# Kernel tuning notes

Hardware: AMD Instinct MI355X
Metric: run time of the kernel (lower is better)

## Reference

```python
import jax, jax.numpy as jnp
import numpy as np

M = 150        # AR2 tail-fit window
LAM = 1e-3     # ridge regularizer in the 2x2 solve
CLIP_K = 4.0   # soft clip multiplier
H = 96         # forecast horizon (base_model.H)


def setup_inputs() -> dict:
    key = jax.random.key(0)
    k1, k2 = jax.random.split(key)
    x = jax.random.normal(k1, (32, 512, 2048), dtype=jnp.float32)
    W = jax.random.normal(k2, (2048, 96), dtype=jnp.float32) * 0.02
    return {"x": x, "W": W}


def _ar2_forecast(x):
    # x: (B, C, L); closed-form AR2 fit on last M samples, vectorized over (B, C)
    y = x[..., -M:]                     # (B, C, M)
    Y = y[..., 2:]                      # targets
    p1 = y[..., 1:-1]
    p2 = y[..., :-2]
    s = lambda a, b: jnp.sum(a * b, axis=-1)
    A11 = s(p1, p1) + LAM
    A22 = s(p2, p2) + LAM
    A12 = s(p1, p2)
    b1 = s(p1, Y)
    b2 = s(p2, Y)
    det = A11 * A22 - A12 * A12
    a1 = (b1 * A22 - b2 * A12) / det    # (B, C)
    a2 = (A11 * b2 - A12 * b1) / det

    def step(carry, _):
        y1, y2 = carry
        yn = a1 * y1 + a2 * y2
        return (yn, y1), yn

    _, out = jax.lax.scan(step, (x[..., -1], x[..., -2]), None, length=H)
    return jnp.moveaxis(out, 0, -1)     # (B, C, H)


def reference(x, W):
    # AR2 part is computed on detached history in the original (numpy round-trip)
    Yb = jax.lax.stop_gradient(_ar2_forecast(x))
    d_hat = jnp.einsum('bcl,lh->bch', x, W)          # base model: per-channel linear head
    y_hat = Yb + d_hat
    last = x[..., -1:]                               # (B, C, 1), broadcasts over H
    hstd = jnp.maximum(jnp.std(x, axis=-1, ddof=1, keepdims=True), 1e-6)  # torch unbiased std
    return jnp.clip(y_hat, last - CLIP_K * hstd, last + CLIP_K * hstd)
```

## Files before the change

kernel.cpp:

```cpp
#include <hip/hip_runtime.h>
#include <math.h>

constexpr int L     = 2048;
constexpr int NH    = 96;
constexpr int MLEN  = 150;
constexpr int NAR   = 148;
constexpr float LAM    = 0.001f;
constexpr float CLIP_K = 4.0f;

constexpr int TM     = 64;
constexpr int KM     = 64;
constexpr int MSTEPS = L / KM;

typedef __attribute__((ext_vector_type(8))) short short8;
typedef __attribute__((ext_vector_type(4))) float floatx4;

__device__ inline short f2bf(float f) {
    union { float f; unsigned u; } v; v.f = f;
    unsigned r = v.u + 0x7FFFu + ((v.u >> 16) & 1u);
    return (short)(r >> 16);
}

__global__ __launch_bounds__(256) void wt_kernel(
    const float* __restrict__ W, short* __restrict__ Wt)
{
    int idx = blockIdx.x * 256 + threadIdx.x;
    int n = idx >> 11;
    int k = idx & 2047;
    Wt[idx] = f2bf(W[k * NH + n]);
}

__global__ __launch_bounds__(512) void gemm_ar2_kernel(
    const float* __restrict__ x, const short* __restrict__ Wt,
    float* __restrict__ out)
{
    __shared__ float As[2][TM * KM];
    __shared__ short Bs[2][NH * KM];
    __shared__ float los[TM], his[TM];

    const int t    = threadIdx.x;
    const int lane = t & 63;
    const int wv   = t >> 6;
    const int h    = wv >> 1;
    const int g    = wv & 1;
    const int m    = lane & 15;
    const int quad = lane >> 4;
    const int row0 = blockIdx.x * TM;
    const int r    = h * 16 + m;
    const int m7   = m & 7;

    const int cA0 = (wv * 2) * 64 + lane, cA1 = cA0 + 64;
    const int rA0 = cA0 >> 4, chA0 = cA0 & 15;
    const int rA1 = cA1 >> 4, chA1 = cA1 & 15;
    const float* pa0 = x + (size_t)(row0 + rA0) * L
                         + ((chA0 >> 3) * 32 + ((chA0 & 7) ^ (rA0 & 7)) * 4);
    const float* pa1 = x + (size_t)(row0 + rA1) * L
                         + ((chA1 >> 3) * 32 + ((chA1 & 7) ^ (rA1 & 7)) * 4);

    const int cB0 = wv * 64 + lane;
    const int cB1 = (8 + wv) * 64 + lane;
    const short* pb0 = Wt + (size_t)(cB0 >> 3) * L + (((cB0 & 7) ^ ((cB0 >> 3) & 7)) * 8);
    const short* pb1 = Wt + (size_t)(cB1 >> 3) * L + (((cB1 & 7) ^ ((cB1 >> 3) & 7)) * 8);

    floatx4 acc[3];
    #pragma unroll
    for (int jj = 0; jj < 3; ++jj) acc[jj] = floatx4{0.f, 0.f, 0.f, 0.f};
    float sum = 0.f, sumsq = 0.f;

    auto stage = [&](int buf, int k0) {
        __builtin_amdgcn_global_load_lds(
            (const __attribute__((address_space(1))) unsigned int*)(pa0 + k0),
            (__attribute__((address_space(3))) unsigned int*)&As[buf][(wv * 2) * 256], 16, 0, 0);
        __builtin_amdgcn_global_load_lds(
            (const __attribute__((address_space(1))) unsigned int*)(pa1 + k0),
            (__attribute__((address_space(3))) unsigned int*)&As[buf][(wv * 2 + 1) * 256], 16, 0, 0);
        __builtin_amdgcn_global_load_lds(
            (const __attribute__((address_space(1))) unsigned int*)(pb0 + k0),
            (__attribute__((address_space(3))) unsigned int*)&Bs[buf][wv * 512], 16, 0, 0);
        if (wv < 4)
            __builtin_amdgcn_global_load_lds(
                (const __attribute__((address_space(1))) unsigned int*)(pb1 + k0),
                (__attribute__((address_space(3))) unsigned int*)&Bs[buf][(8 + wv) * 512], 16, 0, 0);
    };

    stage(0, 0);

    const int pA0 = (2 * quad) ^ m7, pA1 = (2 * quad + 1) ^ m7;

    for (int s = 0; s < MSTEPS; ++s) {
        const int cur = s & 1;
        __syncthreads();
        if (s + 1 < MSTEPS) stage(cur ^ 1, (s + 1) * KM);

        #pragma unroll
        for (int ss = 0; ss < 2; ++ss) {
            float4 f0 = *(const float4*)&As[cur][r * KM + ss * 32 + pA0 * 4];
            float4 f1 = *(const float4*)&As[cur][r * KM + ss * 32 + pA1 * 4];

            if (g == 0) {
                sum  += ((f0.x + f0.y) + (f0.z + f0.w))
                      + ((f1.x + f1.y) + (f1.z + f1.w));
                sumsq = fmaf(f0.x, f0.x, sumsq); sumsq = fmaf(f0.y, f0.y, sumsq);
                sumsq = fmaf(f0.z, f0.z, sumsq); sumsq = fmaf(f0.w, f0.w, sumsq);
                sumsq = fmaf(f1.x, f1.x, sumsq); sumsq = fmaf(f1.y, f1.y, sumsq);
                sumsq = fmaf(f1.z, f1.z, sumsq); sumsq = fmaf(f1.w, f1.w, sumsq);
            }

            short8 af;
            af[0] = f2bf(f0.x); af[1] = f2bf(f0.y); af[2] = f2bf(f0.z); af[3] = f2bf(f0.w);
            af[4] = f2bf(f1.x); af[5] = f2bf(f1.y); af[6] = f2bf(f1.z); af[7] = f2bf(f1.w);

            const int bch = ((ss * 4 + quad) ^ m7) * 8;
            #pragma unroll
            for (int jj = 0; jj < 3; ++jj) {
                short8 bf = *(const short8*)&Bs[cur][(g * 48 + jj * 16 + m) * KM + bch];
                acc[jj] = __builtin_amdgcn_mfma_f32_16x16x32_bf16(af, bf, acc[jj], 0, 0, 0);
            }
        }
    }

    float a1c = 0.f, a2c = 0.f, last = 0.f, y2i = 0.f, lo = 0.f, hi = 0.f;
    if (g == 0) {
        sum   += __shfl_xor(sum,   16); sum   += __shfl_xor(sum,   32);
        sumsq += __shfl_xor(sumsq, 16); sumsq += __shfl_xor(sumsq, 32);

        const float* ytail = x + (size_t)(row0 + r) * L + (L - MLEN);
        float A11 = 0.f, A22 = 0.f, A12 = 0.f, b1 = 0.f, b2 = 0.f;
        for (int i = quad; i < NAR; i += 4) {
            float p2v = ytail[i];
            float p1v = ytail[i + 1];
            float Yv  = ytail[i + 2];
            A11 = fmaf(p1v, p1v, A11);
            A22 = fmaf(p2v, p2v, A22);
            A12 = fmaf(p1v, p2v, A12);
            b1  = fmaf(p1v, Yv,  b1);
            b2  = fmaf(p2v, Yv,  b2);
        }
        A11 += __shfl_xor(A11, 16); A11 += __shfl_xor(A11, 32);
        A22 += __shfl_xor(A22, 16); A22 += __shfl_xor(A22, 32);
        A12 += __shfl_xor(A12, 16); A12 += __shfl_xor(A12, 32);
        b1  += __shfl_xor(b1,  16); b1  += __shfl_xor(b1,  32);
        b2  += __shfl_xor(b2,  16); b2  += __shfl_xor(b2,  32);

        if (quad == 0) {
            A11 += LAM; A22 += LAM;
            float det = A11 * A22 - A12 * A12;
            a1c = (b1 * A22 - b2 * A12) / det;
            a2c = (A11 * b2 - A12 * b1) / det;
            last = ytail[MLEN - 1];
            y2i  = ytail[MLEN - 2];
            float var  = (sumsq - sum * sum * (1.0f / L)) * (1.0f / (L - 1));
            float hstd = fmaxf(sqrtf(fmaxf(var, 0.f)), 1e-6f);
            lo = last - CLIP_K * hstd;
            hi = last + CLIP_K * hstd;
        }
    }
    __syncthreads();

    float* YsF = (float*)As;
    if (g == 0 && quad == 0) {
        float y1 = last, y2 = y2i;
        for (int n = 0; n < NH; ++n) {
            float yn = a1c * y1 + a2c * y2;
            YsF[r * (NH + 1) + n] = yn;
            y2 = y1; y1 = yn;
        }
        los[r] = lo;
        his[r] = hi;
    }
    __syncthreads();

    #pragma unroll
    for (int reg = 0; reg < 4; ++reg) {
        int rl = h * 16 + quad * 4 + reg;
        float rlo = los[rl], rhi = his[rl];
        #pragma unroll
        for (int jj = 0; jj < 3; ++jj) {
            int c = (3 * g + jj) * 16 + m;
            float v = acc[jj][reg] + YsF[rl * (NH + 1) + c];
            v = fminf(fmaxf(v, rlo), rhi);
            out[(size_t)(row0 + rl) * NH + c] = v;
        }
    }
}

extern "C" void kernel_launch(void* const* d_in, const int* in_sizes, int n_in,
                              void* d_out, int out_size, void* d_ws, size_t ws_size,
                              hipStream_t stream) {
    const float* x = (const float*)d_in[0];
    const float* W = (const float*)d_in[1];
    float* out = (float*)d_out;
    short* Wt  = (short*)d_ws;

    wt_kernel<<<dim3((NH * L) / 256), dim3(256), 0, stream>>>(W, Wt);

    const int rows = 32 * 512;
    gemm_ar2_kernel<<<dim3(rows / TM), dim3(512), 0, stream>>>(x, Wt, out);
}
```

Before: 210.3 us.

## Halve GEMM row tile and add triple-buffered LDS pipeline with vmcnt barriers

Shrinks the row tile from 64 to 32 rows per block with 256 threads, doubling the grid to 512 blocks. The LDS buffers go from two stages to three, with prefetch two steps ahead, and a single s_waitcnt vmcnt plus barrier per iteration replaces the __syncthreads-before-stage pattern. The goal is to keep more x loads in flight and to spread work over more CUs, so the memory-bound GEMM streams x faster. In exchange, every W tile is reloaded twice as often per row, and the hand-counted vmcnt(5) must exactly match the five loads issued per stage.

```diff
diff --git a/kernel.cpp b/kernel.cpp
--- a/kernel.cpp
+++ b/kernel.cpp
@@ -8,7 +8,7 @@
 constexpr float LAM    = 0.001f;
 constexpr float CLIP_K = 4.0f;
 
-constexpr int TM     = 64;
+constexpr int TM     = 32;
 constexpr int KM     = 64;
 constexpr int MSTEPS = L / KM;
 
@@ -30,12 +30,12 @@
     Wt[idx] = f2bf(W[k * NH + n]);
 }
 
-__global__ __launch_bounds__(512) void gemm_ar2_kernel(
+__global__ __launch_bounds__(256) void gemm_ar2_kernel(
     const float* __restrict__ x, const short* __restrict__ Wt,
     float* __restrict__ out)
 {
-    __shared__ float As[2][TM * KM];
-    __shared__ short Bs[2][NH * KM];
+    __shared__ float As[3][TM * KM];
+    __shared__ short Bs[3][NH * KM];
     __shared__ float los[TM], his[TM];
 
     const int t    = threadIdx.x;
@@ -49,53 +49,68 @@
     const int r    = h * 16 + m;
     const int m7   = m & 7;
 
-    const int cA0 = (wv * 2) * 64 + lane, cA1 = cA0 + 64;
-    const int rA0 = cA0 >> 4, chA0 = cA0 & 15;
-    const int rA1 = cA1 >> 4, chA1 = cA1 & 15;
-    const float* pa0 = x + (size_t)(row0 + rA0) * L
-                         + ((chA0 >> 3) * 32 + ((chA0 & 7) ^ (rA0 & 7)) * 4);
-    const float* pa1 = x + (size_t)(row0 + rA1) * L
-                         + ((chA1 >> 3) * 32 + ((chA1 & 7) ^ (rA1 & 7)) * 4);
-
-    const int cB0 = wv * 64 + lane;
-    const int cB1 = (8 + wv) * 64 + lane;
-    const short* pb0 = Wt + (size_t)(cB0 >> 3) * L + (((cB0 & 7) ^ ((cB0 >> 3) & 7)) * 8);
-    const short* pb1 = Wt + (size_t)(cB1 >> 3) * L + (((cB1 & 7) ^ ((cB1 >> 3) & 7)) * 8);
+    const float* paSrc[2];
+    int aDst[2];
+    #pragma unroll
+    for (int u = 0; u < 2; ++u) {
+        int i  = wv * 2 + u;
+        int rr = i * 4 + (lane >> 4);
+        int c  = lane & 15;
+        int gg = (c & 8) | ((c ^ (rr & 7)) & 7);
+        paSrc[u] = x + (size_t)(row0 + rr) * L + gg * 4;
+        aDst[u]  = i * 256;
+    }
+
+    const short* pbSrc[3];
+    int bDst[3];
+    #pragma unroll
+    for (int u = 0; u < 3; ++u) {
+        int i  = wv * 3 + u;
+        int nn = i * 8 + (lane >> 3);
+        int c  = lane & 7;
+        int gg = (c ^ (nn & 7)) & 7;
+        pbSrc[u] = Wt + (size_t)nn * L + gg * 8;
+        bDst[u]  = i * 512;
+    }
+
+    auto stage = [&](int buf, int k0) {
+        #pragma unroll
+        for (int u = 0; u < 2; ++u)
+            __builtin_amdgcn_global_load_lds(
+                (const __attribute__((address_space(1))) unsigned int*)(paSrc[u] + k0),
+                (__attribute__((address_space(3))) unsigned int*)&As[buf][aDst[u]], 16, 0, 0);
+        #pragma unroll
+        for (int u = 0; u < 3; ++u)
+            __builtin_amdgcn_global_load_lds(
+                (const __attribute__((address_space(1))) unsigned int*)(pbSrc[u] + k0),
+                (__attribute__((address_space(3))) unsigned int*)&Bs[buf][bDst[u]], 16, 0, 0);
+    };
 
     floatx4 acc[3];
     #pragma unroll
     for (int jj = 0; jj < 3; ++jj) acc[jj] = floatx4{0.f, 0.f, 0.f, 0.f};
     float sum = 0.f, sumsq = 0.f;
 
-    auto stage = [&](int buf, int k0) {
-        __builtin_amdgcn_global_load_lds(
-            (const __attribute__((address_space(1))) unsigned int*)(pa0 + k0),
-            (__attribute__((address_space(3))) unsigned int*)&As[buf][(wv * 2) * 256], 16, 0, 0);
-        __builtin_amdgcn_global_load_lds(
-            (const __attribute__((address_space(1))) unsigned int*)(pa1 + k0),
-            (__attribute__((address_space(3))) unsigned int*)&As[buf][(wv * 2 + 1) * 256], 16, 0, 0);
-        __builtin_amdgcn_global_load_lds(
-            (const __attribute__((address_space(1))) unsigned int*)(pb0 + k0),
-            (__attribute__((address_space(3))) unsigned int*)&Bs[buf][wv * 512], 16, 0, 0);
-        if (wv < 4)
-            __builtin_amdgcn_global_load_lds(
-                (const __attribute__((address_space(1))) unsigned int*)(pb1 + k0),
-                (__attribute__((address_space(3))) unsigned int*)&Bs[buf][(8 + wv) * 512], 16, 0, 0);
-    };
-
     stage(0, 0);
-
-    const int pA0 = (2 * quad) ^ m7, pA1 = (2 * quad + 1) ^ m7;
-
+    stage(1, KM);
+    asm volatile("s_waitcnt vmcnt(5)\n\ts_barrier" ::: "memory");
+
+    int buf = 0;
     for (int s = 0; s < MSTEPS; ++s) {
-        const int cur = s & 1;
-        __syncthreads();
-        if (s + 1 < MSTEPS) stage(cur ^ 1, (s + 1) * KM);
+        const int nb = (buf + 2 >= 3) ? (buf + 2 - 3) : (buf + 2);
+        const int k2 = ((s + 2 < MSTEPS) ? (s + 2) : (MSTEPS - 1)) * KM;
+        stage(nb, k2);
+
+        const float* Ab = &As[buf][0];
+        const short* Bb = &Bs[buf][0];
 
         #pragma unroll
         for (int ss = 0; ss < 2; ++ss) {
-            float4 f0 = *(const float4*)&As[cur][r * KM + ss * 32 + pA0 * 4];
-            float4 f1 = *(const float4*)&As[cur][r * KM + ss * 32 + pA1 * 4];
+            const int ch0 = ss * 8 + 2 * quad;
+            const int p0  = (ch0 & 8) | ((ch0 ^ m7) & 7);
+            const int p1  = ((ch0 + 1) & 8) | (((ch0 + 1) ^ m7) & 7);
+            float4 f0 = *(const float4*)&Ab[r * KM + p0 * 4];
+            float4 f1 = *(const float4*)&Ab[r * KM + p1 * 4];
 
             if (g == 0) {
                 sum  += ((f0.x + f0.y) + (f0.z + f0.w))
@@ -110,14 +125,19 @@
             af[0] = f2bf(f0.x); af[1] = f2bf(f0.y); af[2] = f2bf(f0.z); af[3] = f2bf(f0.w);
             af[4] = f2bf(f1.x); af[5] = f2bf(f1.y); af[6] = f2bf(f1.z); af[7] = f2bf(f1.w);
 
-            const int bch = ((ss * 4 + quad) ^ m7) * 8;
+            const int pb = ((ss * 4 + quad) ^ m7) & 7;
             #pragma unroll
             for (int jj = 0; jj < 3; ++jj) {
-                short8 bf = *(const short8*)&Bs[cur][(g * 48 + jj * 16 + m) * KM + bch];
+                short8 bf = *(const short8*)&Bb[(g * 48 + jj * 16 + m) * KM + pb * 8];
                 acc[jj] = __builtin_amdgcn_mfma_f32_16x16x32_bf16(af, bf, acc[jj], 0, 0, 0);
             }
         }
-    }
+
+        asm volatile("s_waitcnt vmcnt(5)\n\ts_barrier" ::: "memory");
+        buf = (buf + 1 >= 3) ? 0 : (buf + 1);
+    }
+
+    __syncthreads();
 
     float a1c = 0.f, a2c = 0.f, last = 0.f, y2i = 0.f, lo = 0.f, hi = 0.f;
     if (g == 0) {
@@ -155,9 +175,8 @@
             hi = last + CLIP_K * hstd;
         }
     }
-    __syncthreads();
-
-    float* YsF = (float*)As;
+
+    float* YsF = (float*)Bs;
     if (g == 0 && quad == 0) {
         float y1 = last, y2 = y2i;
         for (int n = 0; n < NH; ++n) {
@@ -195,5 +214,5 @@
     wt_kernel<<<dim3((NH * L) / 256), dim3(256), 0, stream>>>(W, Wt);
 
     const int rows = 32 * 512;
-    gemm_ar2_kernel<<<dim3(rows / TM), dim3(512), 0, stream>>>(x, Wt, out);
-}
+    gemm_ar2_kernel<<<dim3(rows / TM), dim3(256), 0, stream>>>(x, Wt, out);
+}
```

New measurement: 208.1 us. Within noise of the previous version (-1.0%).
